# Kernel optimization log

Hardware: AMD Instinct MI355X
Metric: run time of the kernel (lower is better)

The kernel has to match this reference:

```python
import jax, jax.numpy as jnp
import numpy as np
from jax.scipy.special import xlogy

LAMBDA_XM = 0.05
LAMBDA_SEG2D = 1.0
BN_EPS = 1e-5


def setup_inputs() -> dict:
    key = jax.random.key(0)
    ks = jax.random.split(key, 40)
    S, N, Nv, B, Np, M, H, C, MID = 2, 240000, 80000, 2, 120000, 30000, 64, 20, 16
    Nimg = B * M
    f = lambda i, shape, s=0.05: jax.random.normal(ks[i], shape, jnp.float32) * s
    inp = {
        'img_feat': f(0, (S, Nimg, H), 1.0),
        'pts_feat': f(1, (S, Nv, H), 1.0),
        'coors_inv': jax.random.randint(ks[2], (S, N), 0, Nv),
        'labels': jax.random.randint(ks[3], (N,), 0, C),
        'img_label': jax.random.randint(ks[4], (Nimg,), 0, C),
        'p2img_idx': jax.random.randint(ks[5], (B, M), 0, Np),
        # multihead 3d classifiers (per scale): Linear(H,128)-ReLU-Linear(128,C)
        'w3a': f(6, (S, H, 128)), 'b3a': jnp.zeros((S, 128)),
        'w3b': f(7, (S, 128, C)), 'b3b': jnp.zeros((S, C)),
        # multihead fuse classifiers
        'wfa': f(8, (S, H, 128)), 'bfa': jnp.zeros((S, 128)),
        'wfb': f(9, (S, 128, C)), 'bfb': jnp.zeros((S, C)),
        # attention: fc1(H->H//4), fc2(H->H//4), fc3(H//2->2), conv1/conv2 (1x1 -> linear) + BN
        'fc1w': f(10, (S, H, MID)), 'fc1b': jnp.zeros((S, MID)),
        'fc2w': f(11, (S, H, MID)), 'fc2b': jnp.zeros((S, MID)),
        'fc3w': f(12, (S, 2 * MID, 2)), 'fc3b': jnp.zeros((S, 2)),
        'c1w': f(13, (S, H, H)), 'c1b': jnp.zeros((S, H)),
        'bn1g': jnp.ones((S, H)), 'bn1b': jnp.zeros((S, H)),
        'c2w': f(14, (S, H, H)), 'c2b': jnp.zeros((S, H)),
        'bn2g': jnp.ones((S, H)), 'bn2b': jnp.zeros((S, H)),
        # final classifier Linear(S*H,128)-ReLU-Linear(128,C)
        'clw1': f(15, (S * H, 128)), 'clb1': jnp.zeros((128,)),
        'clw2': f(16, (128, C)), 'clb2': jnp.zeros((C,)),
    }
    return inp


def _mlp2(x, w1, b1, w2, b2):
    return jax.nn.relu(x @ w1 + b1) @ w2 + b2


def _ce(logits, lab):
    logp = jax.nn.log_softmax(logits, -1)
    return -jnp.take_along_axis(logp, lab[:, None], axis=1).mean()


def _lovasz(probs, lab):
    # lovasz-softmax over all classes, averaged over present classes
    C = probs.shape[1]
    fg = jax.nn.one_hot(lab, C, dtype=probs.dtype)  # [N,C]
    errors = jnp.abs(fg - probs)

    def per_class(err_c, fg_c):
        order = jnp.argsort(-err_c)
        e = err_c[order]
        f = fg_c[order]
        gts = f.sum()
        inter = gts - jnp.cumsum(f)
        union = gts + jnp.cumsum(1.0 - f)
        jac = 1.0 - inter / union
        jac = jnp.concatenate([jac[:1], jac[1:] - jac[:-1]])
        return jnp.dot(e, jac)

    losses = jax.vmap(per_class)(errors.T, fg.T)  # [C]
    present = (fg.sum(0) > 0).astype(probs.dtype)
    return jnp.sum(losses * present) / jnp.maximum(present.sum(), 1.0)


def _seg_loss(logits, lab):
    return _ce(logits, lab) + _lovasz(jax.nn.softmax(logits, -1), lab)


def _convbn_relu(x, cw, cb, g, b):
    # 1x1 Conv1d == per-point linear; BN (training-mode batch stats over points)
    y = x @ cw + cb
    mu = y.mean(0)
    var = y.var(0)
    return jax.nn.relu((y - mu) * jax.lax.rsqrt(var + BN_EPS) * g + b)


def reference(img_feat, pts_feat, coors_inv, labels, img_label, p2img_idx,
              w3a, b3a, w3b, b3b, wfa, bfa, wfb, bfb,
              fc1w, fc1b, fc2w, fc2b, fc3w, fc3b,
              c1w, c1b, bn1g, bn1b, c2w, c2b, bn2g, bn2b,
              clw1, clb1, clw2, clb2):
    S, Nv, H = pts_feat.shape
    C = w3b.shape[-1]
    B, M = p2img_idx.shape
    N = labels.shape[0]
    Np = N // B
    # p2img_mapping: per-batch gather composed to one global gather (batch blocks are contiguous/equal)
    gidx = (jnp.arange(B)[:, None] * Np + p2img_idx).reshape(-1)  # [Nimg]

    loss = jnp.float32(0.0)
    feats = []
    for s in range(S):
        pred3d = _mlp2(pts_feat[s], w3a[s], b3a[s], w3b[s], b3b[s])  # [Nv,C]
        # voxelize_labels: majority vote per voxel (== unique+scatter_max count argmax)
        counts = jnp.zeros((Nv, C), jnp.float32).at[coors_inv[s], labels].add(1.0)
        vox_lab = jnp.argmax(counts, axis=1)  # [Nv]
        # gather voxel feats/preds to image-projected points (fused gather)
        idx = coors_inv[s][gidx]  # [Nimg]
        p = pts_feat[s][idx]      # [Nimg,H] pseudo feats
        pts_pred = pred3d[idx]    # [Nimg,C]
        v = img_feat[s]           # [Nimg,H] valid (image) feats
        # Attention fusion
        w = jax.nn.sigmoid(
            jnp.concatenate([p @ fc1w[s] + fc1b[s], v @ fc2w[s] + fc2b[s]], -1) @ fc3w[s] + fc3b[s])  # [Nimg,2]
        fuse = (_convbn_relu(p, c1w[s], c1b[s], bn1g[s], bn1b[s]) * w[:, 0:1]
                + _convbn_relu(v, c2w[s], c2b[s], bn2g[s], bn2b[s]) * w[:, 1:2])
        feats.append(fuse)
        fuse_pred = _mlp2(fuse, wfa[s], bfa[s], wfb[s], bfb[s])
        loss = loss + _seg_loss(pred3d, vox_lab)
        loss = loss + _seg_loss(fuse_pred, img_label) * LAMBDA_SEG2D / S
        # F.kl_div(log_softmax(pts_pred), softmax(fuse_pred)), reduction='mean' over all elements
        pf = jax.nn.softmax(fuse_pred, -1)
        kl = jnp.mean(xlogy(pf, pf) - pf * jax.nn.log_softmax(pts_pred, -1))
        loss = loss + kl * LAMBDA_XM / S
    img_logits = _mlp2(jnp.concatenate(feats, -1), clw1, clb1, clw2, clb2)
    loss = loss + _seg_loss(img_logits, img_label)
    return loss
```

## Files before the change

kernel.cpp:

```cpp
#include <hip/hip_runtime.h>
#include <stdint.h>

static constexpr int NV   = 80000;
static constexpr int NPT  = 240000;
static constexpr int NIMG = 60000;
static constexpr int Hh   = 64;
static constexpr int Cc   = 20;
static constexpr int NPp  = 120000;
static constexpr int Mm   = 30000;
static constexpr int NB     = 8192;
static constexpr int NCH    = 16;
static constexpr int NBLK_GA  = (NIMG + 63) / 64;
static constexpr int NBLK_MLP = NV / 64;
static constexpr int NBLK_CNT = (NPT + 255) / 256;
static constexpr int NBLK_FILL_NV = (NV + 255) / 256;
static constexpr int NBLK_HIST = Cc * NCH;
static constexpr int NBLK_GATH = 2 * NIMG * 8 / 256;
static constexpr int NBLK_P3G  = (2 * NIMG + 255) / 256;
#define BN_EPS 1e-5f

using bf16x8 = __attribute__((ext_vector_type(8))) short;
using f32x4  = __attribute__((ext_vector_type(4))) float;

__device__ __forceinline__ float waveReduce(float v) {
  #pragma unroll
  for (int o = 32; o > 0; o >>= 1) v += __shfl_down(v, o);
  return v;
}
__device__ __forceinline__ short f2bf(float f) {
  uint32_t u = __float_as_uint(f);
  return (short)((u + 0x7FFFu + ((u >> 16) & 1u)) >> 16);
}
__device__ __forceinline__ float bf2f(uint32_t h) { return __uint_as_float(h << 16); }
__device__ __forceinline__ uint32_t pk2(float a, float b) {
  return ((uint32_t)(uint16_t)f2bf(a)) | ((uint32_t)(uint16_t)f2bf(b) << 16);
}

struct PackDesc { const float* src; short* dst; int K, Nr, nt; };
struct PackArgs { PackDesc d[14]; };

__global__ void __launch_bounds__(256)
k_pack_zero(PackArgs pa,
            const float* __restrict__ fc1w, const float* __restrict__ fc1b,
            const float* __restrict__ fc2w, const float* __restrict__ fc2b,
            const float* __restrict__ fc3w, const float* __restrict__ fc3b,
            float* __restrict__ attEffs,
            uint4* __restrict__ zb, int zq,
            const int* __restrict__ ci0, const int* __restrict__ ci1,
            const int* __restrict__ p2img,
            int* __restrict__ idx0, int* __restrict__ idx1,
            const float* __restrict__ pts, uint16_t* __restrict__ pgath) {
  int bid = blockIdx.x;
  if (bid >= 384) {
    int g = (bid - 384) * 256 + threadIdx.x;
    int row = g >> 3, q = g & 7;
    int r = (row >= NIMG) ? row - NIMG : row;
    int s1 = (row >= NIMG) ? 1 : 0;
    const int* ci = s1 ? ci1 : ci0;
    int b = (r >= Mm) ? 1 : 0;
    int id = ci[b * NPp + p2img[r]];
    if (q == 0) { if (s1) idx1[r] = id; else idx0[r] = id; }
    const float* src = pts + (size_t)s1 * NV * 64 + (size_t)id * 64 + q * 8;
    float4 a = *(const float4*)src;
    float4 c = *(const float4*)(src + 4);
    uint4 o;
    o.x = pk2(a.x, a.y); o.y = pk2(a.z, a.w);
    o.z = pk2(c.x, c.y); o.w = pk2(c.z, c.w);
    *(uint4*)(pgath + (size_t)row * 64 + q * 8) = o;
    return;
  }
  if (bid >= 128) {
    const uint4 z = make_uint4(0u, 0u, 0u, 0u);
    int i = (bid - 128) * 256 + threadIdx.x;
    for (; i < zq; i += 256 * 256) zb[i] = z;
    return;
  }
  const int stride = 128 * 256;
  for (int di = 0; di < 14; di++) {
    const float* src = pa.d[di].src;
    short* dst = pa.d[di].dst;
    int K = pa.d[di].K, Nr = pa.d[di].Nr, ntiles = pa.d[di].nt;
    int total = (K / 32) * ntiles * 512;
    for (int idx = bid * 256 + threadIdx.x; idx < total; idx += stride) {
      int j = idx & 7, lane = (idx >> 3) & 63, tile = idx >> 9;
      int nt = tile % ntiles, kt = tile / ntiles;
      int k = kt * 32 + (lane >> 4) * 8 + j;
      int n = nt * 16 + (lane & 15);
      float v = (n < Nr) ? src[(size_t)k * Nr + n] : 0.f;
      dst[idx] = f2bf(v);
    }
  }
  if (bid < 2 && threadIdx.x < 64) {
    int s = bid, t = threadIdx.x;
    const float* f1w = fc1w + s * 64 * 16; const float* f1b = fc1b + s * 16;
    const float* f2w = fc2w + s * 64 * 16; const float* f2b = fc2b + s * 16;
    const float* f3w = fc3w + s * 64;      const float* f3b = fc3b + s * 2;
    float* aE = attEffs + s * 320;
    float p0 = 0.f, p1 = 0.f, v0 = 0.f, v1 = 0.f;
    #pragma unroll
    for (int j = 0; j < 16; j++) {
      p0 = fmaf(f1w[t * 16 + j], f3w[j * 2], p0);
      p1 = fmaf(f1w[t * 16 + j], f3w[j * 2 + 1], p1);
      v0 = fmaf(f2w[t * 16 + j], f3w[(16 + j) * 2], v0);
      v1 = fmaf(f2w[t * 16 + j], f3w[(16 + j) * 2 + 1], v1);
    }
    aE[t * 2] = p0; aE[t * 2 + 1] = p1;
    aE[128 + t * 2] = v0; aE[128 + t * 2 + 1] = v1;
    if (t == 0) {
      float b0 = f3b[0], b1 = f3b[1];
      for (int j = 0; j < 16; j++) {
        b0 += f1b[j] * f3w[j * 2] + f2b[j] * f3w[(16 + j) * 2];
        b1 += f1b[j] * f3w[j * 2 + 1] + f2b[j] * f3w[(16 + j) * 2 + 1];
      }
      aE[256] = b0; aE[257] = b1;
    }
  }
}

__device__ void scanbin_body(const unsigned long long* __restrict__ H64,
                             int n, int call, float* __restrict__ lossesC5,
                             int* __restrict__ gts5, int cls) {
  __shared__ int sWC[4], sWF[4];
  __shared__ float sRedF[4];
  int t = threadIdx.x;
  int lane = t & 63, w = t >> 6;
  const uint4* Hv = (const uint4*)(H64 + (size_t)cls * NB + (size_t)t * 32);
  int locC = 0, locF = 0;
  #pragma unroll
  for (int i = 0; i < 16; i++) {
    uint4 u = Hv[i];
    locF += (int)(u.x + u.z);
    locC += (int)(u.y + u.w);
  }
  int sc = locC, sf = locF;
  #pragma unroll
  for (int o = 1; o < 64; o <<= 1) {
    int a = __shfl_up(sc, o);
    int b = __shfl_up(sf, o);
    if (lane >= o) { sc += a; sf += b; }
  }
  if (lane == 63) { sWC[w] = sc; sWF[w] = sf; }
  __syncthreads();
  int offC = 0, offF = 0, Ftot = 0;
  #pragma unroll
  for (int ww = 0; ww < 4; ww++) {
    int fc = sWF[ww];
    Ftot += fc;
    if (ww < w) { offC += sWC[ww]; offF += fc; }
  }
  int runC = offC + sc - locC;
  int runF = offF + sf - locF;
  float gts = (float)Ftot;
  float contrib = 0.f;
  #pragma unroll
  for (int i = 0; i < 16; i++) {
    uint4 u = Hv[i];
    #pragma unroll
    for (int j = 0; j < 2; j++) {
      int cnt = (int)(j ? u.w : u.y), fgc = (int)(j ? u.z : u.x);
      runC += cnt; runF += fgc;
      if (cnt > 0 && Ftot > 0) {
        float r0 = (float)(n - runC);
        float F0 = (float)(Ftot - runF);
        float r1 = r0 + (float)cnt;
        float F1 = F0 + (float)fgc;
        float emean = __uint_as_float((uint32_t)(t * 32 + i * 2 + j) << 17);
        contrib += emean * (r1 / (gts + r1 - F1) - r0 / (gts + r0 - F0));
      }
    }
  }
  contrib = waveReduce(contrib);
  if (lane == 0) sRedF[w] = contrib;
  __syncthreads();
  if (t == 0) {
    lossesC5[call * 32 + cls] = (Ftot > 0) ? (sRedF[0] + sRedF[1] + sRedF[2] + sRedF[3]) : 0.f;
    gts5[call * 32 + cls] = Ftot;
  }
}

__device__ void tile_loss(const float* __restrict__ sL, int r0, int rows, int n,
                          const int* __restrict__ lab, uint16_t* __restrict__ E,
                          float ceScale, float* __restrict__ lossAcc,
                          const float* __restrict__ p3g, float klScale) {
  int t = threadIdx.x;
  if (t < 64) {
    float total = 0.f;
    int gr = r0 + t;
    if (gr < rows) {
      const float* l = sL + t * 21;
      float m = l[0];
      #pragma unroll
      for (int c = 1; c < Cc; c++) m = fmaxf(m, l[c]);
      float ex[Cc]; float se = 0.f;
      #pragma unroll
      for (int c = 0; c < Cc; c++) { ex[c] = expf(l[c] - m); se += ex[c]; }
      float inv = 1.f / se;
      float lse = logf(se);
      int lb = lab[gr];
      total = -(l[lb] - m - lse) * ceScale;
      #pragma unroll
      for (int c = 0; c < Cc; c++) {
        float prob = ex[c] * inv;
        int fg = (c == lb) ? 1 : 0;
        float err = fg ? (1.f - prob) : prob;
        err = fmaxf(err, 0.f);
        uint32_t key = __float_as_uint(err) >> 17;
        E[(size_t)c * n + gr] = (uint16_t)((key << 1) | (uint32_t)fg);
      }
      if (p3g) {
        const float* q = p3g + (size_t)gr * Cc;
        float mq = q[0];
        #pragma unroll
        for (int c = 1; c < Cc; c++) mq = fmaxf(mq, q[c]);
        float sq = 0.f;
        #pragma unroll
        for (int c = 0; c < Cc; c++) sq += expf(q[c] - mq);
        float lsq = logf(sq);
        float kl = 0.f;
        #pragma unroll
        for (int c = 0; c < Cc; c++) {
          float lf = l[c] - m - lse;
          float pf = ex[c] * inv;
          float lq = q[c] - mq - lsq;
          kl += pf * (lf - lq);
        }
        total += kl * klScale;
      }
    }
    total = waveReduce(total);
    if (t == 0) atomicAdd(lossAcc, total);
  }
}

template<int D, bool TO_LDS>
__device__ __forceinline__ void mfma_mlp_core(const short* sXb, short* sH, float* sL,
    int r0, int rows,
    const short* __restrict__ pw1, const float* __restrict__ B1,
    const short* __restrict__ pw2, const float* __restrict__ B2,
    float* __restrict__ Out) {
  constexpr int LDB = D + 8;
  constexpr int KT1 = D / 32;
  const int t = threadIdx.x;
  const int lane = t & 63, w = t >> 6;
  const int m = lane & 15, quad = lane >> 4;
  const int rowA = 16 * w + m;
  bf16x8 a1[KT1];
  #pragma unroll
  for (int kt = 0; kt < KT1; kt++)
    a1[kt] = *(const bf16x8*)(sXb + rowA * LDB + kt * 32 + quad * 8);
  const bf16x8* b1 = (const bf16x8*)pw1;
  #pragma unroll
  for (int nt = 0; nt < 8; nt++) {
    f32x4 c = {0.f, 0.f, 0.f, 0.f};
    #pragma unroll
    for (int kt = 0; kt < KT1; kt++)
      c = __builtin_amdgcn_mfma_f32_16x16x32_bf16(a1[kt], b1[(kt * 8 + nt) * 64 + lane], c, 0, 0, 0);
    int col = nt * 16 + m;
    float bc = B1[col];
    #pragma unroll
    for (int reg = 0; reg < 4; reg++)
      sH[(16 * w + quad * 4 + reg) * 136 + col] = f2bf(fmaxf(c[reg] + bc, 0.f));
  }
  __syncthreads();
  bf16x8 a2[4];
  #pragma unroll
  for (int kt = 0; kt < 4; kt++)
    a2[kt] = *(const bf16x8*)(sH + rowA * 136 + kt * 32 + quad * 8);
  const bf16x8* b2 = (const bf16x8*)pw2;
  #pragma unroll
  for (int nt = 0; nt < 2; nt++) {
    f32x4 c = {0.f, 0.f, 0.f, 0.f};
    #pragma unroll
    for (int kt = 0; kt < 4; kt++)
      c = __builtin_amdgcn_mfma_f32_16x16x32_bf16(a2[kt], b2[(kt * 2 + nt) * 64 + lane], c, 0, 0, 0);
    int col = nt * 16 + m;
    if (col < Cc) {
      float bc = B2[col];
      #pragma unroll
      for (int reg = 0; reg < 4; reg++) {
        int rr = 16 * w + quad * 4 + reg;
        if (TO_LDS) {
          sL[rr * 21 + col] = c[reg] + bc;
        } else {
          int gr = r0 + rr;
          if (gr < rows) Out[(size_t)gr * Cc + col] = c[reg] + bc;
        }
      }
    }
  }
}

__device__ void mlp64_body(int bid0, const float* __restrict__ X,
    const short* __restrict__ pw1, const float* __restrict__ B1,
    const short* __restrict__ pw2, const float* __restrict__ B2,
    float* __restrict__ Out, int rows, char* smem) {
  short* sXb = (short*)smem;
  short* sH  = (short*)(smem + 9216);
  int t = threadIdx.x, r0 = bid0 * 64;
  for (int i = t; i < 1024; i += 256) {
    int r = i >> 4, k4 = (i & 15) * 4;
    int gr = r0 + r;
    float4 v = (gr < rows) ? *(const float4*)(X + (size_t)gr * 64 + k4)
                           : make_float4(0.f, 0.f, 0.f, 0.f);
    uint2 p; p.x = pk2(v.x, v.y); p.y = pk2(v.z, v.w);
    *(uint2*)(sXb + r * 72 + k4) = p;
  }
  __syncthreads();
  mfma_mlp_core<64, false>(sXb, sH, nullptr, r0, rows, pw1, B1, pw2, B2, Out);
}

__device__ void mlp128_loss_body(int bid0, const uint16_t* __restrict__ Xh,
    const short* __restrict__ pw1, const float* __restrict__ B1,
    const short* __restrict__ pw2, const float* __restrict__ B2,
    const int* __restrict__ lab, uint16_t* __restrict__ E, float ce,
    float* __restrict__ lossAcc, char* smem) {
  short* sXb = (short*)smem;
  short* sH  = (short*)(smem + 17408);
  int t = threadIdx.x, r0 = bid0 * 64;
  for (int i = t; i < 2048; i += 256) {
    int r = i >> 5, k4 = (i & 31) * 4;
    int gr = r0 + r;
    uint2 p = (gr < NIMG) ? *(const uint2*)(Xh + (size_t)gr * 128 + k4) : make_uint2(0u, 0u);
    *(uint2*)(sXb + r * 136 + k4) = p;
  }
  __syncthreads();
  mfma_mlp_core<128, true>(sXb, sH, (float*)sXb, r0, NIMG, pw1, B1, pw2, B2, nullptr);
  __syncthreads();
  tile_loss((float*)sXb, r0, NIMG, NIMG, lab, E, ce, lossAcc, nullptr, 0.f);
}

__device__ void cnt_body(int bid0, const int* __restrict__ ci, const int* __restrict__ labels,
                         int* __restrict__ counts) {
  int i = bid0 * 256 + threadIdx.x;
  if (i < NPT) atomicAdd(&counts[(size_t)ci[i] * Cc + labels[i]], 1);
}

__device__ void colred_body(int bid0, const float* __restrict__ partials,
                            float* __restrict__ red64) {
  int t = threadIdx.x, j = bid0;
  float v = 0.f;
  for (int b = j; b < NBLK_GA; b += 64) v += partials[(size_t)b * 256 + t];
  red64[j * 256 + t] = v;
}

__device__ void p3gath_body(int bid0, const float* __restrict__ pred3d0,
                            const float* __restrict__ pred3d1,
                            const int* __restrict__ idx0, const int* __restrict__ idx1,
                            float* __restrict__ p3g0, float* __restrict__ p3g1) {
  int row = bid0 * 256 + threadIdx.x;
  if (row >= 2 * NIMG) return;
  int s1 = (row >= NIMG) ? 1 : 0;
  int r = s1 ? row - NIMG : row;
  const float* pred = s1 ? pred3d1 : pred3d0;
  float* dst = (s1 ? p3g1 : p3g0) + (size_t)r * Cc;
  const float* src = pred + (size_t)(s1 ? idx1[r] : idx0[r]) * Cc;
  #pragma unroll
  for (int c = 0; c < Cc; c += 2) {
    uint2 v = *(const uint2*)(src + c);
    *(uint2*)(dst + c) = v;
  }
}

__device__ void fill_body(int bid0, const float* __restrict__ logits,
                          const int* __restrict__ vcnt,
                          int n, uint16_t* __restrict__ E,
                          float ceScale, float* __restrict__ lossAcc) {
  int i = bid0 * 256 + threadIdx.x;
  float total = 0.f;
  if (i < n) {
    const int* crow = vcnt + (size_t)i * Cc;
    int best = crow[0], lb = 0;
    #pragma unroll
    for (int k = 1; k < Cc; k++) {
      int ck = crow[k];
      if (ck > best) { best = ck; lb = k; }
    }
    const float* l = logits + (size_t)i * Cc;
    float m = l[0];
    #pragma unroll
    for (int c = 1; c < Cc; c++) m = fmaxf(m, l[c]);
    float ex[Cc]; float se = 0.f;
    #pragma unroll
    for (int c = 0; c < Cc; c++) { ex[c] = expf(l[c] - m); se += ex[c]; }
    float inv = 1.f / se;
    float lse = logf(se);
    total = -(l[lb] - m - lse) * ceScale;
    #pragma unroll
    for (int c = 0; c < Cc; c++) {
      float prob = ex[c] * inv;
      int fg = (c == lb) ? 1 : 0;
      float err = fg ? (1.f - prob) : prob;
      err = fmaxf(err, 0.f);
      uint32_t key = __float_as_uint(err) >> 17;
      E[(size_t)c * n + i] = (uint16_t)((key << 1) | (uint32_t)fg);
    }
  }
  total = waveReduce(total);
  __shared__ float sh[4];
  int lane = threadIdx.x & 63, w = threadIdx.x >> 6;
  if (lane == 0) sh[w] = total;
  __syncthreads();
  if (threadIdx.x == 0) atomicAdd(lossAcc, sh[0] + sh[1] + sh[2] + sh[3]);
}

__device__ void hist_body(int bid0, const uint16_t* __restrict__ E, int n,
                          unsigned long long* __restrict__ H64, char* smem) {
  uint32_t* lcf = (uint32_t*)smem;
  int t = threadIdx.x;
  int cls = bid0 / NCH, ch = bid0 - cls * NCH;
  int CHsz = (n + NCH - 1) / NCH;
  int i0 = ch * CHsz;
  int i1 = min(n, i0 + CHsz);
  for (int b = t; b < NB; b += 256) lcf[b] = 0u;
  __syncthreads();
  const uint16_t* Ec = E + (size_t)cls * n;
  for (int i = i0 + t; i < i1; i += 256) {
    uint32_t p = Ec[i];
    atomicAdd(&lcf[p >> 1], 0x10000u | (p & 1u));
  }
  __syncthreads();
  unsigned long long* Hc = H64 + (size_t)cls * NB;
  for (int b = t; b < NB; b += 256) {
    uint32_t v = lcf[b];
    if (v)
      atomicAdd(&Hc[b], ((unsigned long long)(v >> 16) << 32) | (v & 0xFFFFu));
  }
}

__device__ void gatt_body(int bid0, const uint16_t* __restrict__ pg,
                          const float* __restrict__ img,
                          const short* __restrict__ pc1, const float* __restrict__ c1b,
                          const short* __restrict__ pc2, const float* __restrict__ c2b,
                          const float* __restrict__ attEff,
                          uint16_t* __restrict__ y1, uint16_t* __restrict__ y2,
                          float* __restrict__ attw, float* __restrict__ partials,
                          char* smem) {
  short* sP = (short*)smem;
  short* sV = (short*)(smem + 9216);
  float* sAtt  = (float*)(smem + 18432);
  float* sStat = (float*)(smem + 20480);
  int t = threadIdx.x;
  int r0 = bid0 * 64;
  for (int i = t; i < 512; i += 256) {
    int r = i >> 3, q = i & 7;
    int gr = r0 + r;
    uint4 pv = make_uint4(0u, 0u, 0u, 0u);
    if (gr < NIMG) pv = *(const uint4*)(pg + (size_t)gr * 64 + q * 8);
    *(uint4*)(sP + r * 72 + q * 8) = pv;
  }
  for (int i = t; i < 1024; i += 256) {
    int r = i >> 4, q = i & 15;
    int gr = r0 + r;
    float4 vv = make_float4(0.f, 0.f, 0.f, 0.f);
    if (gr < NIMG) vv = *(const float4*)(img + (size_t)gr * 64 + q * 4);
    uint2 qv;
    qv.x = pk2(vv.x, vv.y); qv.y = pk2(vv.z, vv.w);
    *(uint2*)(sV + r * 72 + q * 4) = qv;
  }
  __syncthreads();
  {
    int r = t & 63, qq = t >> 6;
    const float* aP = attEff;
    const float* aV = attEff + 128;
    float l0 = 0.f, l1 = 0.f;
    for (int k = qq * 16; k < qq * 16 + 16; k += 4) {
      uint2 up = *(const uint2*)(sP + r * 72 + k);
      uint2 uv = *(const uint2*)(sV + r * 72 + k);
      float p0 = bf2f(up.x & 0xffff), p1 = bf2f(up.x >> 16);
      float p2 = bf2f(up.y & 0xffff), p3 = bf2f(up.y >> 16);
      float v0 = bf2f(uv.x & 0xffff), v1 = bf2f(uv.x >> 16);
      float v2 = bf2f(uv.y & 0xffff), v3 = bf2f(uv.y >> 16);
      float4 wa = *(const float4*)(aP + 2 * k);
      float4 wb = *(const float4*)(aP + 2 * k + 4);
      l0 += p0 * wa.x + p1 * wa.z + p2 * wb.x + p3 * wb.z;
      l1 += p0 * wa.y + p1 * wa.w + p2 * wb.y + p3 * wb.w;
      float4 ua = *(const float4*)(aV + 2 * k);
      float4 ub = *(const float4*)(aV + 2 * k + 4);
      l0 += v0 * ua.x + v1 * ua.z + v2 * ub.x + v3 * ub.z;
      l1 += v0 * ua.y + v1 * ua.w + v2 * ub.y + v3 * ub.w;
    }
    sAtt[r * 8 + qq * 2] = l0;
    sAtt[r * 8 + qq * 2 + 1] = l1;
  }
  const int lane = t & 63, w = t >> 6;
  const int m = lane & 15, quad = lane >> 4;
  const int rowA = 16 * w + m;
  bf16x8 ap[2], av[2];
  #pragma unroll
  for (int kt = 0; kt < 2; kt++) {
    ap[kt] = *(const bf16x8*)(sP + rowA * 72 + kt * 32 + quad * 8);
    av[kt] = *(const bf16x8*)(sV + rowA * 72 + kt * 32 + quad * 8);
  }
  const bf16x8* b1 = (const bf16x8*)pc1;
  const bf16x8* b2 = (const bf16x8*)pc2;
  #pragma unroll
  for (int nt = 0; nt < 4; nt++) {
    int col = nt * 16 + m;
    f32x4 c1 = {0.f, 0.f, 0.f, 0.f}, c2 = {0.f, 0.f, 0.f, 0.f};
    #pragma unroll
    for (int kt = 0; kt < 2; kt++) {
      c1 = __builtin_amdgcn_mfma_f32_16x16x32_bf16(ap[kt], b1[(kt * 4 + nt) * 64 + lane], c1, 0, 0, 0);
      c2 = __builtin_amdgcn_mfma_f32_16x16x32_bf16(av[kt], b2[(kt * 4 + nt) * 64 + lane], c2, 0, 0, 0);
    }
    float bb1 = c1b[col], bb2 = c2b[col];
    float s1 = 0.f, q1 = 0.f, s2 = 0.f, q2 = 0.f;
    #pragma unroll
    for (int reg = 0; reg < 4; reg++) {
      int gr = r0 + 16 * w + quad * 4 + reg;
      if (gr < NIMG) {
        float v1 = c1[reg] + bb1, v2 = c2[reg] + bb2;
        y1[(size_t)gr * 64 + col] = (uint16_t)f2bf(v1);
        y2[(size_t)gr * 64 + col] = (uint16_t)f2bf(v2);
        s1 += v1; q1 = fmaf(v1, v1, q1);
        s2 += v2; q2 = fmaf(v2, v2, q2);
      }
    }
    s1 += __shfl_down(s1, 32); s1 += __shfl_down(s1, 16);
    q1 += __shfl_down(q1, 32); q1 += __shfl_down(q1, 16);
    s2 += __shfl_down(s2, 32); s2 += __shfl_down(s2, 16);
    q2 += __shfl_down(q2, 32); q2 += __shfl_down(q2, 16);
    if (lane < 16) {
      float* base = sStat + (w * 4 + nt) * 64 + lane;
      base[0]  = s1;
      base[16] = q1;
      base[32] = s2;
      base[48] = q2;
    }
  }
  __syncthreads();
  {
    int kind = t >> 6, col = t & 63;
    int nt = col >> 4, mm = col & 15;
    float v = 0.f;
    #pragma unroll
    for (int ww = 0; ww < 4; ww++)
      v += sStat[(ww * 4 + nt) * 64 + kind * 16 + mm];
    partials[(size_t)bid0 * 256 + kind * 64 + col] = v;
  }
  if (t < 64) {
    int gr = r0 + t;
    if (gr < NIMG) {
      float l0 = attEff[256] + sAtt[t * 8] + sAtt[t * 8 + 2] + sAtt[t * 8 + 4] + sAtt[t * 8 + 6];
      float l1 = attEff[257] + sAtt[t * 8 + 1] + sAtt[t * 8 + 3] + sAtt[t * 8 + 5] + sAtt[t * 8 + 7];
      attw[gr * 2]     = 1.f / (1.f + expf(-l0));
      attw[gr * 2 + 1] = 1.f / (1.f + expf(-l1));
    }
  }
}

__device__ void fusemlp_body(int bid0,
    const uint16_t* __restrict__ y1, const uint16_t* __restrict__ y2,
    const float* __restrict__ attw, const float* __restrict__ red64,
    const float* __restrict__ g1, const float* __restrict__ be1,
    const float* __restrict__ g2, const float* __restrict__ be2,
    uint16_t* __restrict__ feats, int s64,
    const short* __restrict__ pw1, const float* __restrict__ B1,
    const short* __restrict__ pw2, const float* __restrict__ B2,
    const int* __restrict__ lab, uint16_t* __restrict__ E, float ce,
    const float* __restrict__ p3g, float klScale,
    float* __restrict__ lossAcc, char* smem) {
  short* sXb = (short*)smem;
  short* sH  = (short*)(smem + 9216);
  float* sBn = (float*)(smem + 9216 + 17408);
  int t = threadIdx.x, r0 = bid0 * 64;
  float acc = 0.f;
  #pragma unroll 8
  for (int b = 0; b < 64; b++) acc += red64[b * 256 + t];
  float* sSum = (float*)sH;
  sSum[t] = acc;
  __syncthreads();
  if (t < 64) {
    float nn = (float)NIMG;
    float mu1 = sSum[t] / nn;
    float var1 = sSum[64 + t] / nn - mu1 * mu1;
    float a1 = g1[t] / sqrtf(var1 + BN_EPS);
    sBn[t] = a1; sBn[64 + t] = be1[t] - mu1 * a1;
    float mu2 = sSum[128 + t] / nn;
    float var2 = sSum[192 + t] / nn - mu2 * mu2;
    float a2 = g2[t] / sqrtf(var2 + BN_EPS);
    sBn[128 + t] = a2; sBn[192 + t] = be2[t] - mu2 * a2;
  }
  __syncthreads();
  for (int i = t; i < 1024; i += 256) {
    int r = i >> 4, q = i & 15;
    int gr = r0 + r;
    uint2 zp = make_uint2(0u, 0u);
    if (gr < NIMG) {
      float4 a1 = *(const float4*)(sBn + q * 4);
      float4 c1 = *(const float4*)(sBn + 64 + q * 4);
      float4 a2 = *(const float4*)(sBn + 128 + q * 4);
      float4 c2 = *(const float4*)(sBn + 192 + q * 4);
      uint2 u1 = *(const uint2*)(y1 + (size_t)gr * 64 + q * 4);
      uint2 u2 = *(const uint2*)(y2 + (size_t)gr * 64 + q * 4);
      float w0 = attw[gr * 2], w1 = attw[gr * 2 + 1];
      float zx = fmaxf(fmaf(bf2f(u1.x & 0xffff), a1.x, c1.x), 0.f) * w0
               + fmaxf(fmaf(bf2f(u2.x & 0xffff), a2.x, c2.x), 0.f) * w1;
      float zy = fmaxf(fmaf(bf2f(u1.x >> 16),   a1.y, c1.y), 0.f) * w0
               + fmaxf(fmaf(bf2f(u2.x >> 16),   a2.y, c2.y), 0.f) * w1;
      float zz = fmaxf(fmaf(bf2f(u1.y & 0xffff), a1.z, c1.z), 0.f) * w0
               + fmaxf(fmaf(bf2f(u2.y & 0xffff), a2.z, c2.z), 0.f) * w1;
      float zw = fmaxf(fmaf(bf2f(u1.y >> 16),   a1.w, c1.w), 0.f) * w0
               + fmaxf(fmaf(bf2f(u2.y >> 16),   a2.w, c2.w), 0.f) * w1;
      zp.x = pk2(zx, zy); zp.y = pk2(zz, zw);
      *(uint2*)(feats + (size_t)gr * 128 + s64 + q * 4) = zp;
    }
    *(uint2*)(sXb + r * 72 + q * 4) = zp;
  }
  __syncthreads();
  mfma_mlp_core<64, true>(sXb, sH, (float*)sXb, r0, NIMG, pw1, B1, pw2, B2, nullptr);
  __syncthreads();
  tile_loss((float*)sXb, r0, NIMG, NIMG, lab, E, ce, lossAcc, p3g, klScale);
}

__global__ void __launch_bounds__(256)
k_mega2(const float* __restrict__ pf0, const float* __restrict__ pf1,
        const uint16_t* __restrict__ pg0, const uint16_t* __restrict__ pg1,
        const float* __restrict__ if0, const float* __restrict__ if1,
        const short* pc1w0, const short* pc1w1, const short* pc2w0, const short* pc2w1,
        const float* c1b, const float* c2b, const float* attEffs,
        uint16_t* y1a, uint16_t* y2a, uint16_t* y1b, uint16_t* y2b,
        float* attw0, float* attw1, float* partials0, float* partials1,
        const short* pw3a0, const float* b3a, const short* pw3b0, const float* b3b,
        const short* pw3a1, const short* pw3b1,
        float* pred3d0, float* pred3d1,
        const int* __restrict__ ci0, const int* __restrict__ ci1,
        const int* __restrict__ labels,
        int* __restrict__ counts0, int* __restrict__ counts1) {
  __shared__ char smem[26624];
  int bid = blockIdx.x;
  if (bid < NBLK_GA) {
    gatt_body(bid, pg0, if0, pc1w0, c1b, pc2w0, c2b, attEffs,
              y1a, y2a, attw0, partials0, smem);
    return;
  }
  bid -= NBLK_GA;
  if (bid < NBLK_GA) {
    gatt_body(bid, pg1, if1, pc1w1, c1b + 64, pc2w1, c2b + 64, attEffs + 320,
              y1b, y2b, attw1, partials1, smem);
    return;
  }
  bid -= NBLK_GA;
  if (bid < NBLK_MLP) { mlp64_body(bid, pf0, pw3a0, b3a, pw3b0, b3b, pred3d0, NV, smem); return; }
  bid -= NBLK_MLP;
  if (bid < NBLK_MLP) { mlp64_body(bid, pf1, pw3a1, b3a + 128, pw3b1, b3b + Cc, pred3d1, NV, smem); return; }
  bid -= NBLK_MLP;
  if (bid < NBLK_CNT) { cnt_body(bid, ci0, labels, counts0); return; }
  cnt_body(bid - NBLK_CNT, ci1, labels, counts1);
}

__global__ void __launch_bounds__(256)
k_fill_colred(const float* __restrict__ l0, const int* __restrict__ vc0, uint16_t* __restrict__ E0,
              const float* __restrict__ l1, const int* __restrict__ vc1, uint16_t* __restrict__ E1,
              float ce, float* __restrict__ lossAcc,
              const float* partials0, float* red64_0,
              const float* partials1, float* red64_1,
              const int* __restrict__ idx0, const int* __restrict__ idx1,
              float* __restrict__ p3g0, float* __restrict__ p3g1) {
  int bid = blockIdx.x;
  if (bid < NBLK_FILL_NV) {
    fill_body(bid, l0, vc0, NV, E0, ce, lossAcc);
    return;
  }
  bid -= NBLK_FILL_NV;
  if (bid < NBLK_FILL_NV) {
    fill_body(bid, l1, vc1, NV, E1, ce, lossAcc);
    return;
  }
  bid -= NBLK_FILL_NV;
  if (bid < 64) { colred_body(bid, partials0, red64_0); return; }
  bid -= 64;
  if (bid < 64) { colred_body(bid, partials1, red64_1); return; }
  p3gath_body(bid - 64, l0, l1, idx0, idx1, p3g0, p3g1);
}

__global__ void __launch_bounds__(256)
k_fuse2_hist2(const uint16_t* y1a, const uint16_t* y2a, const float* attw0, const float* red64_0,
              const uint16_t* y1b, const uint16_t* y2b, const float* attw1, const float* red64_1,
              const float* bn1g, const float* bn1b, const float* bn2g, const float* bn2b,
              uint16_t* feats,
              const short* pwfa0, const float* bfa, const short* pwfb0, const float* bfb,
              const short* pwfa1, const short* pwfb1,
              const int* __restrict__ img_label, float ce, float kl, float* lossAcc,
              const float* p3g0, uint16_t* E3,
              const float* p3g1, uint16_t* E4,
              const uint16_t* __restrict__ E0, unsigned long long* H0,
              const uint16_t* __restrict__ E1, unsigned long long* H2) {
  __shared__ char smem[32768];
  int bid = blockIdx.x;
  if (bid < NBLK_GA) {
    fusemlp_body(bid, y1a, y2a, attw0, red64_0, bn1g, bn1b, bn2g, bn2b, feats, 0,
                 pwfa0, bfa, pwfb0, bfb,
                 img_label, E3, ce, p3g0, kl, lossAcc, smem);
    return;
  }
  bid -= NBLK_GA;
  if (bid < NBLK_GA) {
    fusemlp_body(bid, y1b, y2b, attw1, red64_1, bn1g + 64, bn1b + 64, bn2g + 64, bn2b + 64,
                 feats, 64, pwfa1, bfa + 128, pwfb1, bfb + Cc,
                 img_label, E4, ce, p3g1, kl, lossAcc, smem);
    return;
  }
  bid -= NBLK_GA;
  if (bid < NBLK_HIST) { hist_body(bid, E0, NV, H0, smem); return; }
  hist_body(bid - NBLK_HIST, E1, NV, H2, smem);
}

__global__ void __launch_bounds__(256)
k_finx2(const uint16_t* __restrict__ feats,
        const short* pcl1, const float* clb1, const short* pcl2, const float* clb2,
        const int* __restrict__ img_label, uint16_t* E2, float ce, float* lossAcc,
        const uint16_t* __restrict__ E3, unsigned long long* H1,
        const uint16_t* __restrict__ E4, unsigned long long* H3,
        const unsigned long long* H0, const unsigned long long* H2,
        float* lossesC5, int* gts5) {
  __shared__ char smem[34816];
  int bid = blockIdx.x;
  if (bid < NBLK_GA) {
    mlp128_loss_body(bid, feats, pcl1, clb1, pcl2, clb2, img_label, E2, ce, lossAcc, smem);
    return;
  }
  bid -= NBLK_GA;
  if (bid < NBLK_HIST) { hist_body(bid, E3, NIMG, H1, smem); return; }
  bid -= NBLK_HIST;
  if (bid < NBLK_HIST) { hist_body(bid, E4, NIMG, H3, smem); return; }
  bid -= NBLK_HIST;
  if (bid < Cc) { scanbin_body(H0, NV, 0, lossesC5, gts5, bid); return; }
  scanbin_body(H2, NV, 2, lossesC5, gts5, bid - Cc);
}

__global__ void __launch_bounds__(256)
k_hist_scan2(const uint16_t* __restrict__ E2, unsigned long long* H4,
             const unsigned long long* H1, const unsigned long long* H3,
             float* lossesC5, int* gts5) {
  __shared__ char smem[32768];
  int bid = blockIdx.x;
  if (bid < NBLK_HIST) { hist_body(bid, E2, NIMG, H4, smem); return; }
  bid -= NBLK_HIST;
  if (bid < Cc) { scanbin_body(H1, NIMG, 1, lossesC5, gts5, bid); return; }
  scanbin_body(H3, NIMG, 3, lossesC5, gts5, bid - Cc);
}

__global__ void __launch_bounds__(256)
k_scanbin5(const unsigned long long* H64, int n, int call,
           float* lossesC5, int* gts5) {
  scanbin_body(H64, n, call, lossesC5, gts5, blockIdx.x);
}

__global__ void k_final(const float* __restrict__ lossAcc,
                        const float* __restrict__ lossesC5, const int* __restrict__ gts5,
                        float* __restrict__ out) {
  const float coefs[5] = {1.0f, 0.5f, 1.0f, 0.5f, 1.0f};
  float loss = lossAcc[0];
  for (int call = 0; call < 5; call++) {
    float s = 0.f; int np = 0;
    for (int c = 0; c < Cc; c++)
      if (gts5[call * 32 + c] > 0) { s += lossesC5[call * 32 + c]; np++; }
    loss += coefs[call] * s / (float)(np > 0 ? np : 1);
  }
  out[0] = loss;
}

extern "C" void kernel_launch(void* const* d_in, const int* in_sizes, int n_in,
                              void* d_out, int out_size, void* d_ws, size_t ws_size,
                              hipStream_t stream) {
  const float* img_feat = (const float*)d_in[0];
  const float* pts_feat = (const float*)d_in[1];
  const int* coors_inv  = (const int*)d_in[2];
  const int* labels     = (const int*)d_in[3];
  const int* img_label  = (const int*)d_in[4];
  const int* p2img      = (const int*)d_in[5];
  const float* w3a = (const float*)d_in[6];
  const float* b3a = (const float*)d_in[7];
  const float* w3b = (const float*)d_in[8];
  const float* b3b = (const float*)d_in[9];
  const float* wfa = (const float*)d_in[10];
  const float* bfa = (const float*)d_in[11];
  const float* wfb = (const float*)d_in[12];
  const float* bfb = (const float*)d_in[13];
  const float* fc1w = (const float*)d_in[14];
  const float* fc1b = (const float*)d_in[15];
  const float* fc2w = (const float*)d_in[16];
  const float* fc2b = (const float*)d_in[17];
  const float* fc3w = (const float*)d_in[18];
  const float* fc3b = (const float*)d_in[19];
  const float* c1w  = (const float*)d_in[20];
  const float* c1b  = (const float*)d_in[21];
  const float* bn1g = (const float*)d_in[22];
  const float* bn1b = (const float*)d_in[23];
  const float* c2w  = (const float*)d_in[24];
  const float* c2b  = (const float*)d_in[25];
  const float* bn2g = (const float*)d_in[26];
  const float* bn2b = (const float*)d_in[27];
  const float* clw1 = (const float*)d_in[28];
  const float* clb1 = (const float*)d_in[29];
  const float* clw2 = (const float*)d_in[30];
  const float* clb2 = (const float*)d_in[31];
  (void)in_sizes; (void)n_in; (void)out_size; (void)ws_size;

  char* ws = (char*)d_ws;
  size_t off = 0;
  auto alloc = [&](size_t bytes) { void* p = ws + off; off += (bytes + 255) & ~(size_t)255; return p; };
  uint16_t* feats = (uint16_t*)alloc((size_t)NIMG * 128 * 2);
  uint16_t* pgath = (uint16_t*)alloc((size_t)2 * NIMG * 64 * 2);
  float* pred3d0 = (float*)alloc((size_t)NV * Cc * 4);
  float* pred3d1 = (float*)alloc((size_t)NV * Cc * 4);
  float* p3g0 = (float*)alloc((size_t)NIMG * Cc * 4);
  float* p3g1 = (float*)alloc((size_t)NIMG * Cc * 4);
  int* idx0 = (int*)alloc((size_t)NIMG * 4);
  int* idx1 = (int*)alloc((size_t)NIMG * 4);
  uint16_t* y1a = (uint16_t*)alloc((size_t)NIMG * Hh * 2);
  uint16_t* y2a = (uint16_t*)alloc((size_t)NIMG * Hh * 2);
  uint16_t* y1b = (uint16_t*)alloc((size_t)NIMG * Hh * 2);
  uint16_t* y2b = (uint16_t*)alloc((size_t)NIMG * Hh * 2);
  uint16_t* E0 = (uint16_t*)alloc((size_t)Cc * NV * 2);
  uint16_t* E1 = (uint16_t*)alloc((size_t)Cc * NV * 2);
  uint16_t* E2 = (uint16_t*)alloc((size_t)Cc * NIMG * 2);
  uint16_t* E3 = (uint16_t*)alloc((size_t)Cc * NIMG * 2);
  uint16_t* E4 = (uint16_t*)alloc((size_t)Cc * NIMG * 2);
  float* partials0 = (float*)alloc((size_t)NBLK_GA * 256 * 4);
  float* partials1 = (float*)alloc((size_t)NBLK_GA * 256 * 4);
  float* red64_0 = (float*)alloc(64 * 256 * 4);
  float* red64_1 = (float*)alloc(64 * 256 * 4);
  float* attw0 = (float*)alloc((size_t)NIMG * 2 * 4);
  float* attw1 = (float*)alloc((size_t)NIMG * 2 * 4);
  short* pwAll = (short*)alloc(86016 * 2);
  short* pw3a0 = pwAll,          * pw3a1 = pwAll + 8192;
  short* pwfa0 = pwAll + 16384,  * pwfa1 = pwAll + 24576;
  short* pw3b0 = pwAll + 32768,  * pw3b1 = pwAll + 36864;
  short* pwfb0 = pwAll + 40960,  * pwfb1 = pwAll + 45056;
  short* pcl1  = pwAll + 49152;
  short* pcl2  = pwAll + 65536;
  short* pc1w0 = pwAll + 69632,  * pc1w1 = pwAll + 73728;
  short* pc2w0 = pwAll + 77824,  * pc2w1 = pwAll + 81920;
  float* attEffs = (float*)alloc(2 * 320 * 4);
  size_t zsize = 1024 + (size_t)5 * Cc * NB * 8 + (size_t)2 * NV * Cc * 4;
  char* zbase = (char*)alloc(zsize);
  float* lossAcc  = (float*)zbase;
  float* lossesC5 = (float*)zbase + 32;
  int*   gts5     = (int*)((float*)zbase + 192);
  unsigned long long* Hbase = (unsigned long long*)(zbase + 1024);
  auto Hc = [&](int call) { return Hbase + (size_t)call * Cc * NB; };
  int* counts0 = (int*)(zbase + 1024 + (size_t)5 * Cc * NB * 8);
  int* counts1 = counts0 + (size_t)NV * Cc;
  int zq = (int)(zsize / 16);

  const float kl = 0.025f / ((float)NIMG * Cc);
  const float* pf0 = pts_feat;
  const float* pf1 = pts_feat + (size_t)NV * Hh;
  const float* if0 = img_feat;
  const float* if1 = img_feat + (size_t)NIMG * Hh;
  const int* ci0 = coors_inv;
  const int* ci1 = coors_inv + NPT;
  uint16_t* pg0 = pgath;
  uint16_t* pg1 = pgath + (size_t)NIMG * 64;

  PackArgs pa;
  pa.d[0]  = {w3a,        pw3a0, 64, 128, 8};
  pa.d[1]  = {w3a + 8192, pw3a1, 64, 128, 8};
  pa.d[2]  = {wfa,        pwfa0, 64, 128, 8};
  pa.d[3]  = {wfa + 8192, pwfa1, 64, 128, 8};
  pa.d[4]  = {w3b,        pw3b0, 128, 20, 2};
  pa.d[5]  = {w3b + 2560, pw3b1, 128, 20, 2};
  pa.d[6]  = {wfb,        pwfb0, 128, 20, 2};
  pa.d[7]  = {wfb + 2560, pwfb1, 128, 20, 2};
  pa.d[8]  = {clw1,       pcl1, 128, 128, 8};
  pa.d[9]  = {clw2,       pcl2, 128, 20, 2};
  pa.d[10] = {c1w,        pc1w0, 64, 64, 4};
  pa.d[11] = {c1w + 4096, pc1w1, 64, 64, 4};
  pa.d[12] = {c2w,        pc2w0, 64, 64, 4};
  pa.d[13] = {c2w + 4096, pc2w1, 64, 64, 4};
  k_pack_zero<<<384 + NBLK_GATH, 256, 0, stream>>>(
      pa, fc1w, fc1b, fc2w, fc2b, fc3w, fc3b, attEffs,
      (uint4*)zbase, zq, ci0, ci1, p2img, idx0, idx1, pts_feat, pgath);

  k_mega2<<<2 * NBLK_GA + 2 * NBLK_MLP + 2 * NBLK_CNT, 256, 0, stream>>>(
      pf0, pf1, pg0, pg1, if0, if1,
      pc1w0, pc1w1, pc2w0, pc2w1, c1b, c2b, attEffs,
      y1a, y2a, y1b, y2b, attw0, attw1, partials0, partials1,
      pw3a0, b3a, pw3b0, b3b, pw3a1, pw3b1, pred3d0, pred3d1,
      ci0, ci1, labels, counts0, counts1);

  k_fill_colred<<<2 * NBLK_FILL_NV + 128 + NBLK_P3G, 256, 0, stream>>>(
      pred3d0, counts0, E0, pred3d1, counts1, E1, 1.0f / NV, lossAcc,
      partials0, red64_0, partials1, red64_1,
      idx0, idx1, p3g0, p3g1);

  k_fuse2_hist2<<<2 * NBLK_GA + 2 * NBLK_HIST, 256, 0, stream>>>(
      y1a, y2a, attw0, red64_0, y1b, y2b, attw1, red64_1,
      bn1g, bn1b, bn2g, bn2b, feats,
      pwfa0, bfa, pwfb0, bfb, pwfa1, pwfb1,
      img_label, 0.5f / NIMG, kl, lossAcc,
      p3g0, E3, p3g1, E4,
      E0, Hc(0), E1, Hc(2));

  k_finx2<<<NBLK_GA + 2 * NBLK_HIST + 2 * Cc, 256, 0, stream>>>(
      feats, pcl1, clb1, pcl2, clb2,
      img_label, E2, 1.0f / NIMG, lossAcc,
      E3, Hc(1), E4, Hc(3),
      Hc(0), Hc(2), lossesC5, gts5);

  k_hist_scan2<<<NBLK_HIST + 2 * Cc, 256, 0, stream>>>(
      E2, Hc(4), Hc(1), Hc(3), lossesC5, gts5);

  k_scanbin5<<<Cc, 256, 0, stream>>>(Hc(4), NIMG, 4, lossesC5, gts5);

  k_final<<<1, 1, 0, stream>>>(lossAcc, lossesC5, gts5, (float*)d_out);
}
```

Measured before the change: 356.6 us.

## Split fused MLP+loss tail into separate full-width fill passes

The per-tile loss (CE, Lovasz error keys, KL) previously ran on only 64 of 256 threads after each MLP tile. It now moves out of the MLP kernels: logits are written to global buffers and a later fill kernel processes them with one row per thread. The kernel sequence is reshuffled so the fill for the fusion heads runs alongside the final classifier, and the histogram for those heads runs next to the final fill. The cost is an extra global round-trip of NIMG×20 floats for each of three logit sets, plus one more kernel launch.

```diff
diff --git a/kernel.cpp b/kernel.cpp
--- a/kernel.cpp
+++ b/kernel.cpp
@@ -14,6 +14,7 @@
 static constexpr int NBLK_MLP = NV / 64;
 static constexpr int NBLK_CNT = (NPT + 255) / 256;
 static constexpr int NBLK_FILL_NV = (NV + 255) / 256;
+static constexpr int NBLK_FILL_NI = (NIMG + 255) / 256;
 static constexpr int NBLK_HIST = Cc * NCH;
 static constexpr int NBLK_GATH = 2 * NIMG * 8 / 256;
 static constexpr int NBLK_P3G  = (2 * NIMG + 255) / 256;
@@ -178,62 +179,8 @@
   }
 }
 
-__device__ void tile_loss(const float* __restrict__ sL, int r0, int rows, int n,
-                          const int* __restrict__ lab, uint16_t* __restrict__ E,
-                          float ceScale, float* __restrict__ lossAcc,
-                          const float* __restrict__ p3g, float klScale) {
-  int t = threadIdx.x;
-  if (t < 64) {
-    float total = 0.f;
-    int gr = r0 + t;
-    if (gr < rows) {
-      const float* l = sL + t * 21;
-      float m = l[0];
-      #pragma unroll
-      for (int c = 1; c < Cc; c++) m = fmaxf(m, l[c]);
-      float ex[Cc]; float se = 0.f;
-      #pragma unroll
-      for (int c = 0; c < Cc; c++) { ex[c] = expf(l[c] - m); se += ex[c]; }
-      float inv = 1.f / se;
-      float lse = logf(se);
-      int lb = lab[gr];
-      total = -(l[lb] - m - lse) * ceScale;
-      #pragma unroll
-      for (int c = 0; c < Cc; c++) {
-        float prob = ex[c] * inv;
-        int fg = (c == lb) ? 1 : 0;
-        float err = fg ? (1.f - prob) : prob;
-        err = fmaxf(err, 0.f);
-        uint32_t key = __float_as_uint(err) >> 17;
-        E[(size_t)c * n + gr] = (uint16_t)((key << 1) | (uint32_t)fg);
-      }
-      if (p3g) {
-        const float* q = p3g + (size_t)gr * Cc;
-        float mq = q[0];
-        #pragma unroll
-        for (int c = 1; c < Cc; c++) mq = fmaxf(mq, q[c]);
-        float sq = 0.f;
-        #pragma unroll
-        for (int c = 0; c < Cc; c++) sq += expf(q[c] - mq);
-        float lsq = logf(sq);
-        float kl = 0.f;
-        #pragma unroll
-        for (int c = 0; c < Cc; c++) {
-          float lf = l[c] - m - lse;
-          float pf = ex[c] * inv;
-          float lq = q[c] - mq - lsq;
-          kl += pf * (lf - lq);
-        }
-        total += kl * klScale;
-      }
-    }
-    total = waveReduce(total);
-    if (t == 0) atomicAdd(lossAcc, total);
-  }
-}
-
-template<int D, bool TO_LDS>
-__device__ __forceinline__ void mfma_mlp_core(const short* sXb, short* sH, float* sL,
+template<int D>
+__device__ __forceinline__ void mfma_mlp_body(const short* sXb, short* sH,
     int r0, int rows,
     const short* __restrict__ pw1, const float* __restrict__ B1,
     const short* __restrict__ pw2, const float* __restrict__ B2,
@@ -278,13 +225,8 @@
       float bc = B2[col];
       #pragma unroll
       for (int reg = 0; reg < 4; reg++) {
-        int rr = 16 * w + quad * 4 + reg;
-        if (TO_LDS) {
-          sL[rr * 21 + col] = c[reg] + bc;
-        } else {
-          int gr = r0 + rr;
-          if (gr < rows) Out[(size_t)gr * Cc + col] = c[reg] + bc;
-        }
+        int gr = r0 + 16 * w + quad * 4 + reg;
+        if (gr < rows) Out[(size_t)gr * Cc + col] = c[reg] + bc;
       }
     }
   }
@@ -306,14 +248,13 @@
     *(uint2*)(sXb + r * 72 + k4) = p;
   }
   __syncthreads();
-  mfma_mlp_core<64, false>(sXb, sH, nullptr, r0, rows, pw1, B1, pw2, B2, Out);
-}
-
-__device__ void mlp128_loss_body(int bid0, const uint16_t* __restrict__ Xh,
+  mfma_mlp_body<64>(sXb, sH, r0, rows, pw1, B1, pw2, B2, Out);
+}
+
+__device__ void mlp128_body(int bid0, const uint16_t* __restrict__ Xh,
     const short* __restrict__ pw1, const float* __restrict__ B1,
     const short* __restrict__ pw2, const float* __restrict__ B2,
-    const int* __restrict__ lab, uint16_t* __restrict__ E, float ce,
-    float* __restrict__ lossAcc, char* smem) {
+    float* __restrict__ Out, char* smem) {
   short* sXb = (short*)smem;
   short* sH  = (short*)(smem + 17408);
   int t = threadIdx.x, r0 = bid0 * 64;
@@ -324,9 +265,7 @@
     *(uint2*)(sXb + r * 136 + k4) = p;
   }
   __syncthreads();
-  mfma_mlp_core<128, true>(sXb, sH, (float*)sXb, r0, NIMG, pw1, B1, pw2, B2, nullptr);
-  __syncthreads();
-  tile_loss((float*)sXb, r0, NIMG, NIMG, lab, E, ce, lossAcc, nullptr, 0.f);
+  mfma_mlp_body<128>(sXb, sH, r0, NIMG, pw1, B1, pw2, B2, Out);
 }
 
 __device__ void cnt_body(int bid0, const int* __restrict__ ci, const int* __restrict__ labels,
@@ -362,18 +301,25 @@
 }
 
 __device__ void fill_body(int bid0, const float* __restrict__ logits,
-                          const int* __restrict__ vcnt,
+                          const int* __restrict__ lab, const int* __restrict__ vcnt,
                           int n, uint16_t* __restrict__ E,
-                          float ceScale, float* __restrict__ lossAcc) {
+                          float ceScale, float* __restrict__ lossAcc,
+                          const float* __restrict__ p3g, float klScale) {
   int i = bid0 * 256 + threadIdx.x;
   float total = 0.f;
   if (i < n) {
-    const int* crow = vcnt + (size_t)i * Cc;
-    int best = crow[0], lb = 0;
-    #pragma unroll
-    for (int k = 1; k < Cc; k++) {
-      int ck = crow[k];
-      if (ck > best) { best = ck; lb = k; }
+    int lb;
+    if (vcnt) {
+      const int* crow = vcnt + (size_t)i * Cc;
+      int best = crow[0], arg = 0;
+      #pragma unroll
+      for (int k = 1; k < Cc; k++) {
+        int ck = crow[k];
+        if (ck > best) { best = ck; arg = k; }
+      }
+      lb = arg;
+    } else {
+      lb = lab[i];
     }
     const float* l = logits + (size_t)i * Cc;
     float m = l[0];
@@ -393,6 +339,25 @@
       err = fmaxf(err, 0.f);
       uint32_t key = __float_as_uint(err) >> 17;
       E[(size_t)c * n + i] = (uint16_t)((key << 1) | (uint32_t)fg);
+    }
+    if (p3g) {
+      const float* q = p3g + (size_t)i * Cc;
+      float mq = q[0];
+      #pragma unroll
+      for (int c = 1; c < Cc; c++) mq = fmaxf(mq, q[c]);
+      float sq = 0.f;
+      #pragma unroll
+      for (int c = 0; c < Cc; c++) sq += expf(q[c] - mq);
+      float lsq = logf(sq);
+      float kl = 0.f;
+      #pragma unroll
+      for (int c = 0; c < Cc; c++) {
+        float lf = l[c] - m - lse;
+        float pf = ex[c] * inv;
+        float lq = q[c] - mq - lsq;
+        kl += pf * (lf - lq);
+      }
+      total += kl * klScale;
     }
   }
   total = waveReduce(total);
@@ -556,9 +521,7 @@
     uint16_t* __restrict__ feats, int s64,
     const short* __restrict__ pw1, const float* __restrict__ B1,
     const short* __restrict__ pw2, const float* __restrict__ B2,
-    const int* __restrict__ lab, uint16_t* __restrict__ E, float ce,
-    const float* __restrict__ p3g, float klScale,
-    float* __restrict__ lossAcc, char* smem) {
+    float* __restrict__ Out, char* smem) {
   short* sXb = (short*)smem;
   short* sH  = (short*)(smem + 9216);
   float* sBn = (float*)(smem + 9216 + 17408);
@@ -607,9 +570,7 @@
     *(uint2*)(sXb + r * 72 + q * 4) = zp;
   }
   __syncthreads();
-  mfma_mlp_core<64, true>(sXb, sH, (float*)sXb, r0, NIMG, pw1, B1, pw2, B2, nullptr);
-  __syncthreads();
-  tile_loss((float*)sXb, r0, NIMG, NIMG, lab, E, ce, lossAcc, p3g, klScale);
+  mfma_mlp_body<64>(sXb, sH, r0, NIMG, pw1, B1, pw2, B2, Out);
 }
 
 __global__ void __launch_bounds__(256)
@@ -658,12 +619,12 @@
               float* __restrict__ p3g0, float* __restrict__ p3g1) {
   int bid = blockIdx.x;
   if (bid < NBLK_FILL_NV) {
-    fill_body(bid, l0, vc0, NV, E0, ce, lossAcc);
+    fill_body(bid, l0, nullptr, vc0, NV, E0, ce, lossAcc, nullptr, 0.f);
     return;
   }
   bid -= NBLK_FILL_NV;
   if (bid < NBLK_FILL_NV) {
-    fill_body(bid, l1, vc1, NV, E1, ce, lossAcc);
+    fill_body(bid, l1, nullptr, vc1, NV, E1, ce, lossAcc, nullptr, 0.f);
     return;
   }
   bid -= NBLK_FILL_NV;
@@ -680,24 +641,20 @@
               uint16_t* feats,
               const short* pwfa0, const float* bfa, const short* pwfb0, const float* bfb,
               const short* pwfa1, const short* pwfb1,
-              const int* __restrict__ img_label, float ce, float kl, float* lossAcc,
-              const float* p3g0, uint16_t* E3,
-              const float* p3g1, uint16_t* E4,
+              float* fusepred0, float* fusepred1,
               const uint16_t* __restrict__ E0, unsigned long long* H0,
               const uint16_t* __restrict__ E1, unsigned long long* H2) {
   __shared__ char smem[32768];
   int bid = blockIdx.x;
   if (bid < NBLK_GA) {
     fusemlp_body(bid, y1a, y2a, attw0, red64_0, bn1g, bn1b, bn2g, bn2b, feats, 0,
-                 pwfa0, bfa, pwfb0, bfb,
-                 img_label, E3, ce, p3g0, kl, lossAcc, smem);
+                 pwfa0, bfa, pwfb0, bfb, fusepred0, smem);
     return;
   }
   bid -= NBLK_GA;
   if (bid < NBLK_GA) {
     fusemlp_body(bid, y1b, y2b, attw1, red64_1, bn1g + 64, bn1b + 64, bn2g + 64, bn2b + 64,
-                 feats, 64, pwfa1, bfa + 128, pwfb1, bfb + Cc,
-                 img_label, E4, ce, p3g1, kl, lossAcc, smem);
+                 feats, 64, pwfa1, bfa + 128, pwfb1, bfb + Cc, fusepred1, smem);
     return;
   }
   bid -= NBLK_GA;
@@ -708,24 +665,42 @@
 __global__ void __launch_bounds__(256)
 k_finx2(const uint16_t* __restrict__ feats,
         const short* pcl1, const float* clb1, const short* pcl2, const float* clb2,
-        const int* __restrict__ img_label, uint16_t* E2, float ce, float* lossAcc,
-        const uint16_t* __restrict__ E3, unsigned long long* H1,
-        const uint16_t* __restrict__ E4, unsigned long long* H3,
+        float* finalpred,
+        const float* fusepred0, const float* p3g0, uint16_t* E3,
+        const float* fusepred1, const float* p3g1, uint16_t* E4,
+        const int* __restrict__ img_label, float ce, float kl, float* lossAcc,
         const unsigned long long* H0, const unsigned long long* H2,
         float* lossesC5, int* gts5) {
   __shared__ char smem[34816];
   int bid = blockIdx.x;
-  if (bid < NBLK_GA) {
-    mlp128_loss_body(bid, feats, pcl1, clb1, pcl2, clb2, img_label, E2, ce, lossAcc, smem);
-    return;
-  }
+  if (bid < NBLK_GA) { mlp128_body(bid, feats, pcl1, clb1, pcl2, clb2, finalpred, smem); return; }
   bid -= NBLK_GA;
+  if (bid < NBLK_FILL_NI) {
+    fill_body(bid, fusepred0, img_label, nullptr, NIMG, E3, ce, lossAcc, p3g0, kl);
+    return;
+  }
+  bid -= NBLK_FILL_NI;
+  if (bid < NBLK_FILL_NI) {
+    fill_body(bid, fusepred1, img_label, nullptr, NIMG, E4, ce, lossAcc, p3g1, kl);
+    return;
+  }
+  bid -= NBLK_FILL_NI;
+  if (bid < Cc) { scanbin_body(H0, NV, 0, lossesC5, gts5, bid); return; }
+  scanbin_body(H2, NV, 2, lossesC5, gts5, bid - Cc);
+}
+
+__global__ void __launch_bounds__(256)
+k_hist2_fill(const uint16_t* __restrict__ E3, unsigned long long* H1,
+             const uint16_t* __restrict__ E4, unsigned long long* H3,
+             const float* __restrict__ finalpred, const int* __restrict__ img_label,
+             uint16_t* __restrict__ E2, float ce, float* lossAcc) {
+  __shared__ char smem[32768];
+  int bid = blockIdx.x;
   if (bid < NBLK_HIST) { hist_body(bid, E3, NIMG, H1, smem); return; }
   bid -= NBLK_HIST;
   if (bid < NBLK_HIST) { hist_body(bid, E4, NIMG, H3, smem); return; }
-  bid -= NBLK_HIST;
-  if (bid < Cc) { scanbin_body(H0, NV, 0, lossesC5, gts5, bid); return; }
-  scanbin_body(H2, NV, 2, lossesC5, gts5, bid - Cc);
+  fill_body(bid - NBLK_HIST, finalpred, img_label, nullptr, NIMG, E2, ce, lossAcc,
+            nullptr, 0.f);
 }
 
 __global__ void __launch_bounds__(256)
@@ -823,6 +798,9 @@
   float* red64_1 = (float*)alloc(64 * 256 * 4);
   float* attw0 = (float*)alloc((size_t)NIMG * 2 * 4);
   float* attw1 = (float*)alloc((size_t)NIMG * 2 * 4);
+  float* fusepred0 = (float*)alloc((size_t)NIMG * Cc * 4);
+  float* fusepred1 = (float*)alloc((size_t)NIMG * Cc * 4);
+  float* finalpred = (float*)alloc((size_t)NIMG * Cc * 4);
   short* pwAll = (short*)alloc(86016 * 2);
   short* pw3a0 = pwAll,          * pw3a1 = pwAll + 8192;
   short* pwfa0 = pwAll + 16384,  * pwfa1 = pwAll + 24576;
@@ -888,16 +866,19 @@
   k_fuse2_hist2<<<2 * NBLK_GA + 2 * NBLK_HIST, 256, 0, stream>>>(
       y1a, y2a, attw0, red64_0, y1b, y2b, attw1, red64_1,
       bn1g, bn1b, bn2g, bn2b, feats,
-      pwfa0, bfa, pwfb0, bfb, pwfa1, pwfb1,
+      pwfa0, bfa, pwfb0, bfb, pwfa1, pwfb1, fusepred0, fusepred1,
+      E0, Hc(0), E1, Hc(2));
+
+  k_finx2<<<NBLK_GA + 2 * NBLK_FILL_NI + 2 * Cc, 256, 0, stream>>>(
+      feats, pcl1, clb1, pcl2, clb2, finalpred,
+      fusepred0, p3g0, E3,
+      fusepred1, p3g1, E4,
       img_label, 0.5f / NIMG, kl, lossAcc,
-      p3g0, E3, p3g1, E4,
-      E0, Hc(0), E1, Hc(2));
-
-  k_finx2<<<NBLK_GA + 2 * NBLK_HIST + 2 * Cc, 256, 0, stream>>>(
-      feats, pcl1, clb1, pcl2, clb2,
-      img_label, E2, 1.0f / NIMG, lossAcc,
+      Hc(0), Hc(2), lossesC5, gts5);
+
+  k_hist2_fill<<<2 * NBLK_HIST + NBLK_FILL_NI, 256, 0, stream>>>(
       E3, Hc(1), E4, Hc(3),
-      Hc(0), Hc(2), lossesC5, gts5);
+      finalpred, img_label, E2, 1.0f / NIMG, lossAcc);
 
   k_hist_scan2<<<NBLK_HIST + 2 * Cc, 256, 0, stream>>>(
       E2, Hc(4), Hc(1), Hc(3), lossesC5, gts5);
```

New measurement: 349.5 us. -2.0%, faster.
